# Optimization experiments

Measured on AMD Instinct MI355X. Metric: run time of the kernel, lower is better.

## Reference

```python
import jax, jax.numpy as jnp
import numpy as np

T, H, I, E, TOP_K = 1024, 2048, 1024, 32, 2
ROUTED_SCALING = 1.0


def setup_inputs() -> dict:
    key = jax.random.key(0)
    k0, k1, k2, k3, k4 = jax.random.split(key, 5)
    scale_h = 1.0 / np.sqrt(H)
    scale_i = 1.0 / np.sqrt(I)
    return {
        "x": jax.random.normal(k0, (T, H), dtype=jnp.float32),
        "gate_w": jax.random.normal(k1, (E, H), dtype=jnp.float32) * scale_h,      # router: Linear(H, E, bias=False)
        "gate_proj_w": jax.random.normal(k2, (E, I, H), dtype=jnp.float32) * scale_h,
        "up_proj_w": jax.random.normal(k3, (E, I, H), dtype=jnp.float32) * scale_h,
        "down_proj_w": jax.random.normal(k4, (E, H, I), dtype=jnp.float32) * scale_i,
    }


def reference(x, gate_w, gate_proj_w, up_proj_w, down_proj_w):
    # Router: logits [T, E] -> softmax -> top-k -> renormalize over selected experts
    logits = jnp.einsum("th,eh->te", x, gate_w)
    probs = jax.nn.softmax(logits, axis=-1)
    topk_vals, topk_idx = jax.lax.top_k(probs, TOP_K)            # [T, K]
    topk_w = topk_vals / jnp.sum(topk_vals, axis=-1, keepdims=True)
    topk_w = topk_w * ROUTED_SCALING
    # Dense combine weights [T, E]: zero for unselected experts
    onehot = jax.nn.one_hot(topk_idx, E, dtype=x.dtype)          # [T, K, E]
    combine = jnp.einsum("tk,tke->te", topk_w, onehot)           # [T, E]
    # Expert SwiGLU MLP computed densely, masked/weighted by combine weights
    g = jnp.einsum("th,eih->tei", x, gate_proj_w)                # [T, E, I]
    u = jnp.einsum("th,eih->tei", x, up_proj_w)                  # [T, E, I]
    h = jax.nn.silu(g) * u                                        # [T, E, I]
    h = h * combine[:, :, None]                                   # weight before down_proj
    out = jnp.einsum("tei,ehi->th", h, down_proj_w)              # [T, H]
    return out
```

## Files before the change

### kernel.cpp

```cpp
#include <hip/hip_runtime.h>
#include <hip/hip_bf16.h>

#define T_TOK 1024
#define H_DIM 2048
#define I_DIM 1024
#define NE 32

typedef __attribute__((ext_vector_type(8))) short bf16x8_t;
typedef __attribute__((ext_vector_type(4))) float f32x4_t;

__device__ __forceinline__ unsigned short f2bf(float f) {
    unsigned int u = __builtin_bit_cast(unsigned int, f);
    u += 0x7fffu + ((u >> 16) & 1u);
    return (unsigned short)(u >> 16);
}

__device__ __forceinline__ ushort4 f42bf(float4 v) {
    ushort4 r; r.x = f2bf(v.x); r.y = f2bf(v.y); r.z = f2bf(v.z); r.w = f2bf(v.w);
    return r;
}

__global__ __launch_bounds__(256) void moe_router(
    const float* __restrict__ x, const float* __restrict__ gwr,
    int* __restrict__ counts, int* __restrict__ etok, float* __restrict__ ew)
{
    const int t = blockIdx.x;
    const int e = threadIdx.x >> 3;
    const int j = threadIdx.x & 7;
    const float* xr = x + (size_t)t * H_DIM;
    const float* wr = gwr + (size_t)e * H_DIM;
    double s = 0.0;
    for (int c = j * 4; c < H_DIM; c += 32) {
        float4 a = *(const float4*)(xr + c);
        float4 b = *(const float4*)(wr + c);
        s += (double)a.x * b.x + (double)a.y * b.y + (double)a.z * b.z + (double)a.w * b.w;
    }
    s += __shfl_down(s, 4, 8);
    s += __shfl_down(s, 2, 8);
    s += __shfl_down(s, 1, 8);
    __shared__ float lg[NE];
    if (j == 0) lg[e] = (float)s;
    __syncthreads();
    if (threadIdx.x == 0) {
        float l1 = -1e30f, l2 = -1e30f; int i1 = 0, i2 = 0;
        for (int k = 0; k < NE; k++) {
            float v = lg[k];
            if (v > l1) { l2 = l1; i2 = i1; l1 = v; i1 = k; }
            else if (v > l2) { l2 = v; i2 = k; }
        }
        float w2 = 1.f / (1.f + __expf(l1 - l2));
        float w1 = 1.f - w2;
        int p1 = atomicAdd(&counts[i1], 1);
        etok[i1 * T_TOK + p1] = (t << 1);
        ew[i1 * T_TOK + p1] = w1;
        int p2 = atomicAdd(&counts[i2], 1);
        etok[i2 * T_TOK + p2] = (t << 1) | 1;
        ew[i2 * T_TOK + p2] = w2;
    }
}

__global__ __launch_bounds__(512, 2) void moe_gateup(
    const float* __restrict__ x,
    const float* __restrict__ gw,
    const float* __restrict__ uw,
    const int* __restrict__ counts,
    const int* __restrict__ etok,
    const float* __restrict__ ew,
    unsigned short* __restrict__ hbuf)
{
    __shared__ __align__(16) unsigned char smem[67584];
    unsigned short* As = (unsigned short*)smem;
    unsigned short* Gs = (unsigned short*)(smem + 18432);
    unsigned short* Us = (unsigned short*)(smem + 36864);
    float* GL = (float*)smem;

    const int e   = blockIdx.y;
    const int i0  = blockIdx.x * 128;
    const int cnt = counts[e];
    const int tid = threadIdx.x;
    const int wid = tid >> 6, lane = tid & 63;
    const int wm = wid >> 2, wn = wid & 3;
    const int lrow = lane & 15, quad = lane >> 4;

    const unsigned short* Bsrc = (wn < 2) ? Gs : Us;
    const int bro = (wn & 1) * 64;

    for (int m0 = 0; m0 < cnt; m0 += 128) {
        f32x4_t acc[4][4];
        #pragma unroll
        for (int a = 0; a < 4; a++)
            #pragma unroll
            for (int b = 0; b < 4; b++) acc[a][b] = (f32x4_t){0.f, 0.f, 0.f, 0.f};

        for (int k0 = 0; k0 < H_DIM; k0 += 64) {
            __syncthreads();
            #pragma unroll
            for (int i = 0; i < 4; i++) {
                int idx = tid + i * 512;
                int row = idx >> 4, c4 = idx & 15;
                int m = m0 + row;
                int tok = (m < cnt) ? (etok[e * T_TOK + m] >> 1) : 0;
                float4 v = *(const float4*)(x + (size_t)tok * H_DIM + k0 + c4 * 4);
                *(ushort4*)(As + row * 72 + c4 * 4) = f42bf(v);
            }
            #pragma unroll
            for (int i = 0; i < 4; i++) {
                int idx = tid + i * 512;
                int row = idx >> 4, c4 = idx & 15;
                float4 v = *(const float4*)(gw + ((size_t)e * I_DIM + i0 + row) * H_DIM + k0 + c4 * 4);
                *(ushort4*)(Gs + row * 72 + c4 * 4) = f42bf(v);
            }
            #pragma unroll
            for (int i = 0; i < 4; i++) {
                int idx = tid + i * 512;
                int row = idx >> 4, c4 = idx & 15;
                float4 v = *(const float4*)(uw + ((size_t)e * I_DIM + i0 + row) * H_DIM + k0 + c4 * 4);
                *(ushort4*)(Us + row * 72 + c4 * 4) = f42bf(v);
            }
            __syncthreads();
            #pragma unroll
            for (int kk = 0; kk < 2; kk++) {
                bf16x8_t af[4], bfr[4];
                #pragma unroll
                for (int q = 0; q < 4; q++)
                    af[q] = *(const bf16x8_t*)(As + (wm * 64 + q * 16 + lrow) * 72 + kk * 32 + quad * 8);
                #pragma unroll
                for (int q = 0; q < 4; q++)
                    bfr[q] = *(const bf16x8_t*)(Bsrc + (bro + q * 16 + lrow) * 72 + kk * 32 + quad * 8);
                #pragma unroll
                for (int a = 0; a < 4; a++)
                    #pragma unroll
                    for (int b = 0; b < 4; b++)
                        acc[a][b] = __builtin_amdgcn_mfma_f32_16x16x32_bf16(af[a], bfr[b], acc[a][b], 0, 0, 0);
            }
        }
        __syncthreads();
        if (wn < 2) {
            #pragma unroll
            for (int a = 0; a < 4; a++)
                #pragma unroll
                for (int b = 0; b < 4; b++)
                    #pragma unroll
                    for (int r = 0; r < 4; r++) {
                        int row = wm * 64 + a * 16 + quad * 4 + r;
                        int col = wn * 64 + b * 16 + lrow;
                        GL[row * 132 + col] = acc[a][b][r];
                    }
        }
        __syncthreads();
        if (wn >= 2) {
            #pragma unroll
            for (int a = 0; a < 4; a++)
                #pragma unroll
                for (int r = 0; r < 4; r++) {
                    int row = wm * 64 + a * 16 + quad * 4 + r;
                    int m = m0 + row;
                    if (m < cnt) {
                        int ent = etok[e * T_TOK + m];
                        float w = ew[e * T_TOK + m];
                        #pragma unroll
                        for (int b = 0; b < 4; b++) {
                            int colI = (wn - 2) * 64 + b * 16 + lrow;
                            float g = GL[row * 132 + colI];
                            float u = acc[a][b][r];
                            float hv = g / (1.f + __expf(-g)) * u * w;
                            hbuf[(size_t)ent * I_DIM + i0 + colI] = f2bf(hv);
                        }
                    }
                }
        }
    }
}

__global__ __launch_bounds__(512, 2) void moe_down(
    const unsigned short* __restrict__ hbuf,
    const float* __restrict__ dw,
    const int* __restrict__ counts,
    const int* __restrict__ etok,
    float* __restrict__ out)
{
    __shared__ __align__(16) unsigned char smem[55296];
    unsigned short* As = (unsigned short*)smem;
    unsigned short* Ds = (unsigned short*)(smem + 18432);

    const int e   = blockIdx.y;
    const int n0  = blockIdx.x * 256;
    const int cnt = counts[e];
    const int tid = threadIdx.x;
    const int wid = tid >> 6, lane = tid & 63;
    const int wm = wid >> 2, wn = wid & 3;
    const int lrow = lane & 15, quad = lane >> 4;

    for (int m0 = 0; m0 < cnt; m0 += 128) {
        f32x4_t acc[4][4];
        #pragma unroll
        for (int a = 0; a < 4; a++)
            #pragma unroll
            for (int b = 0; b < 4; b++) acc[a][b] = (f32x4_t){0.f, 0.f, 0.f, 0.f};

        for (int k0 = 0; k0 < I_DIM; k0 += 64) {
            __syncthreads();
            #pragma unroll
            for (int i = 0; i < 2; i++) {
                int idx = tid + i * 512;
                int row = idx >> 3, c8 = idx & 7;
                int m = m0 + row;
                int ent = (m < cnt) ? etok[e * T_TOK + m] : 0;
                uint4 v = *(const uint4*)(hbuf + (size_t)ent * I_DIM + k0 + c8 * 8);
                *(uint4*)(As + row * 72 + c8 * 8) = v;
            }
            #pragma unroll
            for (int i = 0; i < 8; i++) {
                int idx = tid + i * 512;
                int row = idx >> 4, c4 = idx & 15;
                float4 v = *(const float4*)(dw + ((size_t)e * H_DIM + n0 + row) * I_DIM + k0 + c4 * 4);
                *(ushort4*)(Ds + row * 72 + c4 * 4) = f42bf(v);
            }
            __syncthreads();
            #pragma unroll
            for (int kk = 0; kk < 2; kk++) {
                bf16x8_t af[4], bfr[4];
                #pragma unroll
                for (int q = 0; q < 4; q++)
                    af[q] = *(const bf16x8_t*)(As + (wm * 64 + q * 16 + lrow) * 72 + kk * 32 + quad * 8);
                #pragma unroll
                for (int q = 0; q < 4; q++)
                    bfr[q] = *(const bf16x8_t*)(Ds + (wn * 64 + q * 16 + lrow) * 72 + kk * 32 + quad * 8);
                #pragma unroll
                for (int a = 0; a < 4; a++)
                    #pragma unroll
                    for (int b = 0; b < 4; b++)
                        acc[a][b] = __builtin_amdgcn_mfma_f32_16x16x32_bf16(af[a], bfr[b], acc[a][b], 0, 0, 0);
            }
        }
        #pragma unroll
        for (int a = 0; a < 4; a++)
            #pragma unroll
            for (int r = 0; r < 4; r++) {
                int row = wm * 64 + a * 16 + quad * 4 + r;
                int m = m0 + row;
                if (m < cnt) {
                    int tok = etok[e * T_TOK + m] >> 1;
                    float* orow = out + (size_t)tok * H_DIM + n0 + wn * 64;
                    #pragma unroll
                    for (int b = 0; b < 4; b++)
                        atomicAdd(orow + b * 16 + lrow, acc[a][b][r]);
                }
            }
    }
}

extern "C" void kernel_launch(void* const* d_in, const int* in_sizes, int n_in,
                              void* d_out, int out_size, void* d_ws, size_t ws_size,
                              hipStream_t stream) {
    const float* x   = (const float*)d_in[0];
    const float* gwr = (const float*)d_in[1];
    const float* gw  = (const float*)d_in[2];
    const float* uw  = (const float*)d_in[3];
    const float* dw  = (const float*)d_in[4];
    float* out = (float*)d_out;

    char* ws = (char*)d_ws;
    int*   counts = (int*)ws;
    int*   etok   = (int*)(ws + 4096);
    float* ew     = (float*)(ws + 4096 + 131072);
    unsigned short* hbuf = (unsigned short*)(ws + 4096 + 262144);

    hipMemsetAsync(counts, 0, 128, stream);
    hipMemsetAsync(d_out, 0, (size_t)out_size * sizeof(float), stream);

    moe_router<<<T_TOK, 256, 0, stream>>>(x, gwr, counts, etok, ew);
    moe_gateup<<<dim3(I_DIM / 128, NE), 512, 0, stream>>>(x, gw, uw, counts, etok, ew, hbuf);
    moe_down<<<dim3(H_DIM / 256, NE), 512, 0, stream>>>(hbuf, dw, counts, etok, out);
}
```

Measured before the change: 882.0 us.

## Double-buffer MoE GEMM tiles with register prefetch and halve tile width

Both expert GEMM kernels now prefetch the next K-slice into registers while MFMAs run on the current LDS buffer, then convert and store into an alternate LDS buffer, using one barrier per step. Tile widths are halved (64 intermediate columns for gate/up, 128 hidden columns for down), which doubles the grid and gives better CU coverage. The aim is to hide global load latency and raise occupancy in this bandwidth-bound workload. In exchange, activation rows are re-read by more blocks, and larger LDS plus tighter launch bounds may raise register pressure.

Measured after the change: 828.0 us. 6.1% less time.

```diff
diff --git a/kernel.cpp b/kernel.cpp
--- a/kernel.cpp
+++ b/kernel.cpp
@@ -59,7 +59,7 @@
     }
 }
 
-__global__ __launch_bounds__(512, 2) void moe_gateup(
+__global__ __launch_bounds__(512, 4) void moe_gateup(
     const float* __restrict__ x,
     const float* __restrict__ gw,
     const float* __restrict__ uw,
@@ -68,183 +68,213 @@
     const float* __restrict__ ew,
     unsigned short* __restrict__ hbuf)
 {
-    __shared__ __align__(16) unsigned char smem[67584];
-    unsigned short* As = (unsigned short*)smem;
-    unsigned short* Gs = (unsigned short*)(smem + 18432);
-    unsigned short* Us = (unsigned short*)(smem + 36864);
-    float* GL = (float*)smem;
-
+    __shared__ __align__(16) unsigned char smem[73728];
     const int e   = blockIdx.y;
-    const int i0  = blockIdx.x * 128;
+    const int i0  = blockIdx.x * 64;
     const int cnt = counts[e];
     const int tid = threadIdx.x;
     const int wid = tid >> 6, lane = tid & 63;
-    const int wm = wid >> 2, wn = wid & 3;
+    const int wm = wid >> 1, wn = wid & 1;
     const int lrow = lane & 15, quad = lane >> 4;
 
-    const unsigned short* Bsrc = (wn < 2) ? Gs : Us;
-    const int bro = (wn & 1) * 64;
+    const float* gbase = gw + ((size_t)e * I_DIM + i0 + (tid >> 4)) * H_DIM + (tid & 15) * 4;
+    const float* ubase = uw + ((size_t)e * I_DIM + i0 + (tid >> 4)) * H_DIM + (tid & 15) * 4;
 
     for (int m0 = 0; m0 < cnt; m0 += 128) {
-        f32x4_t acc[4][4];
-        #pragma unroll
-        for (int a = 0; a < 4; a++)
-            #pragma unroll
-            for (int b = 0; b < 4; b++) acc[a][b] = (f32x4_t){0.f, 0.f, 0.f, 0.f};
-
-        for (int k0 = 0; k0 < H_DIM; k0 += 64) {
+        const float* arow[4];
+        #pragma unroll
+        for (int i = 0; i < 4; i++) {
+            int idx = tid + i * 512;
+            int m = m0 + (idx >> 4);
+            int tok = (m < cnt) ? (etok[e * T_TOK + m] >> 1) : 0;
+            arow[i] = x + (size_t)tok * H_DIM + (idx & 15) * 4;
+        }
+
+        f32x4_t acc[2][4];
+        #pragma unroll
+        for (int a = 0; a < 2; a++)
+            #pragma unroll
+            for (int c = 0; c < 4; c++) acc[a][c] = (f32x4_t){0.f, 0.f, 0.f, 0.f};
+
+        float4 ra[4], rg[2], ru[2];
+        auto load_t = [&](int k0) {
+            #pragma unroll
+            for (int i = 0; i < 4; i++) ra[i] = *(const float4*)(arow[i] + k0);
+            #pragma unroll
+            for (int i = 0; i < 2; i++) rg[i] = *(const float4*)(gbase + (size_t)i * 32 * H_DIM + k0);
+            #pragma unroll
+            for (int i = 0; i < 2; i++) ru[i] = *(const float4*)(ubase + (size_t)i * 32 * H_DIM + k0);
+        };
+        auto store_t = [&](int b) {
+            unsigned short* As = (unsigned short*)(smem + b * 36864);
+            unsigned short* Gs = As + 9216;
+            unsigned short* Us = As + 13824;
+            #pragma unroll
+            for (int i = 0; i < 4; i++) { int idx = tid + i * 512; *(ushort4*)(As + (idx >> 4) * 72 + (idx & 15) * 4) = f42bf(ra[i]); }
+            #pragma unroll
+            for (int i = 0; i < 2; i++) { int idx = tid + i * 512; *(ushort4*)(Gs + (idx >> 4) * 72 + (idx & 15) * 4) = f42bf(rg[i]); }
+            #pragma unroll
+            for (int i = 0; i < 2; i++) { int idx = tid + i * 512; *(ushort4*)(Us + (idx >> 4) * 72 + (idx & 15) * 4) = f42bf(ru[i]); }
+        };
+        auto mm = [&](int b) {
+            const unsigned short* As = (const unsigned short*)(smem + b * 36864);
+            const unsigned short* Bs = As + 9216 + wn * 4608;
+            #pragma unroll
+            for (int kk = 0; kk < 2; kk++) {
+                bf16x8_t af[2], bfr[4];
+                #pragma unroll
+                for (int q = 0; q < 2; q++)
+                    af[q] = *(const bf16x8_t*)(As + (wm * 32 + q * 16 + lrow) * 72 + kk * 32 + quad * 8);
+                #pragma unroll
+                for (int q = 0; q < 4; q++)
+                    bfr[q] = *(const bf16x8_t*)(Bs + (q * 16 + lrow) * 72 + kk * 32 + quad * 8);
+                #pragma unroll
+                for (int a = 0; a < 2; a++)
+                    #pragma unroll
+                    for (int c = 0; c < 4; c++)
+                        acc[a][c] = __builtin_amdgcn_mfma_f32_16x16x32_bf16(af[a], bfr[c], acc[a][c], 0, 0, 0);
+            }
+        };
+
+        load_t(0);
+        store_t(0);
+        __syncthreads();
+        for (int k = 0; k < 32; k++) {
+            if (k < 31) load_t((k + 1) * 64);
+            mm(k & 1);
+            if (k < 31) store_t((k + 1) & 1);
             __syncthreads();
-            #pragma unroll
-            for (int i = 0; i < 4; i++) {
-                int idx = tid + i * 512;
-                int row = idx >> 4, c4 = idx & 15;
-                int m = m0 + row;
-                int tok = (m < cnt) ? (etok[e * T_TOK + m] >> 1) : 0;
-                float4 v = *(const float4*)(x + (size_t)tok * H_DIM + k0 + c4 * 4);
-                *(ushort4*)(As + row * 72 + c4 * 4) = f42bf(v);
-            }
-            #pragma unroll
-            for (int i = 0; i < 4; i++) {
-                int idx = tid + i * 512;
-                int row = idx >> 4, c4 = idx & 15;
-                float4 v = *(const float4*)(gw + ((size_t)e * I_DIM + i0 + row) * H_DIM + k0 + c4 * 4);
-                *(ushort4*)(Gs + row * 72 + c4 * 4) = f42bf(v);
-            }
-            #pragma unroll
-            for (int i = 0; i < 4; i++) {
-                int idx = tid + i * 512;
-                int row = idx >> 4, c4 = idx & 15;
-                float4 v = *(const float4*)(uw + ((size_t)e * I_DIM + i0 + row) * H_DIM + k0 + c4 * 4);
-                *(ushort4*)(Us + row * 72 + c4 * 4) = f42bf(v);
-            }
-            __syncthreads();
-            #pragma unroll
-            for (int kk = 0; kk < 2; kk++) {
-                bf16x8_t af[4], bfr[4];
-                #pragma unroll
-                for (int q = 0; q < 4; q++)
-                    af[q] = *(const bf16x8_t*)(As + (wm * 64 + q * 16 + lrow) * 72 + kk * 32 + quad * 8);
-                #pragma unroll
-                for (int q = 0; q < 4; q++)
-                    bfr[q] = *(const bf16x8_t*)(Bsrc + (bro + q * 16 + lrow) * 72 + kk * 32 + quad * 8);
-                #pragma unroll
-                for (int a = 0; a < 4; a++)
-                    #pragma unroll
-                    for (int b = 0; b < 4; b++)
-                        acc[a][b] = __builtin_amdgcn_mfma_f32_16x16x32_bf16(af[a], bfr[b], acc[a][b], 0, 0, 0);
-            }
-        }
-        __syncthreads();
-        if (wn < 2) {
-            #pragma unroll
-            for (int a = 0; a < 4; a++)
-                #pragma unroll
-                for (int b = 0; b < 4; b++)
+        }
+
+        float* GL = (float*)smem;
+        if (wn == 0) {
+            #pragma unroll
+            for (int a = 0; a < 2; a++)
+                #pragma unroll
+                for (int c = 0; c < 4; c++)
                     #pragma unroll
                     for (int r = 0; r < 4; r++) {
-                        int row = wm * 64 + a * 16 + quad * 4 + r;
-                        int col = wn * 64 + b * 16 + lrow;
-                        GL[row * 132 + col] = acc[a][b][r];
+                        int row = wm * 32 + a * 16 + quad * 4 + r;
+                        GL[row * 68 + c * 16 + lrow] = acc[a][c][r];
                     }
         }
         __syncthreads();
-        if (wn >= 2) {
-            #pragma unroll
-            for (int a = 0; a < 4; a++)
+        if (wn == 1) {
+            #pragma unroll
+            for (int a = 0; a < 2; a++)
                 #pragma unroll
                 for (int r = 0; r < 4; r++) {
-                    int row = wm * 64 + a * 16 + quad * 4 + r;
+                    int row = wm * 32 + a * 16 + quad * 4 + r;
                     int m = m0 + row;
                     if (m < cnt) {
                         int ent = etok[e * T_TOK + m];
                         float w = ew[e * T_TOK + m];
                         #pragma unroll
-                        for (int b = 0; b < 4; b++) {
-                            int colI = (wn - 2) * 64 + b * 16 + lrow;
-                            float g = GL[row * 132 + colI];
-                            float u = acc[a][b][r];
+                        for (int c = 0; c < 4; c++) {
+                            int colI = c * 16 + lrow;
+                            float g = GL[row * 68 + colI];
+                            float u = acc[a][c][r];
                             float hv = g / (1.f + __expf(-g)) * u * w;
                             hbuf[(size_t)ent * I_DIM + i0 + colI] = f2bf(hv);
                         }
                     }
                 }
         }
+        __syncthreads();
     }
 }
 
-__global__ __launch_bounds__(512, 2) void moe_down(
+__global__ __launch_bounds__(512, 4) void moe_down(
     const unsigned short* __restrict__ hbuf,
     const float* __restrict__ dw,
     const int* __restrict__ counts,
     const int* __restrict__ etok,
     float* __restrict__ out)
 {
-    __shared__ __align__(16) unsigned char smem[55296];
-    unsigned short* As = (unsigned short*)smem;
-    unsigned short* Ds = (unsigned short*)(smem + 18432);
-
+    __shared__ __align__(16) unsigned char smem[73728];
     const int e   = blockIdx.y;
-    const int n0  = blockIdx.x * 256;
+    const int n0  = blockIdx.x * 128;
     const int cnt = counts[e];
     const int tid = threadIdx.x;
     const int wid = tid >> 6, lane = tid & 63;
-    const int wm = wid >> 2, wn = wid & 3;
+    const int wm = wid >> 1, wn = wid & 1;
     const int lrow = lane & 15, quad = lane >> 4;
 
+    const float* dbase = dw + ((size_t)e * H_DIM + n0 + (tid >> 4)) * I_DIM + (tid & 15) * 4;
+
     for (int m0 = 0; m0 < cnt; m0 += 128) {
-        f32x4_t acc[4][4];
-        #pragma unroll
-        for (int a = 0; a < 4; a++)
-            #pragma unroll
-            for (int b = 0; b < 4; b++) acc[a][b] = (f32x4_t){0.f, 0.f, 0.f, 0.f};
-
-        for (int k0 = 0; k0 < I_DIM; k0 += 64) {
-            __syncthreads();
-            #pragma unroll
-            for (int i = 0; i < 2; i++) {
-                int idx = tid + i * 512;
-                int row = idx >> 3, c8 = idx & 7;
-                int m = m0 + row;
-                int ent = (m < cnt) ? etok[e * T_TOK + m] : 0;
-                uint4 v = *(const uint4*)(hbuf + (size_t)ent * I_DIM + k0 + c8 * 8);
-                *(uint4*)(As + row * 72 + c8 * 8) = v;
-            }
-            #pragma unroll
-            for (int i = 0; i < 8; i++) {
-                int idx = tid + i * 512;
-                int row = idx >> 4, c4 = idx & 15;
-                float4 v = *(const float4*)(dw + ((size_t)e * H_DIM + n0 + row) * I_DIM + k0 + c4 * 4);
-                *(ushort4*)(Ds + row * 72 + c4 * 4) = f42bf(v);
-            }
-            __syncthreads();
+        const unsigned short* arow[2];
+        #pragma unroll
+        for (int i = 0; i < 2; i++) {
+            int idx = tid + i * 512;
+            int m = m0 + (idx >> 3);
+            int ent = (m < cnt) ? etok[e * T_TOK + m] : 0;
+            arow[i] = hbuf + (size_t)ent * I_DIM + (idx & 7) * 8;
+        }
+
+        f32x4_t acc[2][4];
+        #pragma unroll
+        for (int a = 0; a < 2; a++)
+            #pragma unroll
+            for (int c = 0; c < 4; c++) acc[a][c] = (f32x4_t){0.f, 0.f, 0.f, 0.f};
+
+        uint4 raa[2]; float4 rd[4];
+        auto load_t = [&](int k0) {
+            #pragma unroll
+            for (int i = 0; i < 2; i++) raa[i] = *(const uint4*)(arow[i] + k0);
+            #pragma unroll
+            for (int i = 0; i < 4; i++) rd[i] = *(const float4*)(dbase + (size_t)i * 32 * I_DIM + k0);
+        };
+        auto store_t = [&](int b) {
+            unsigned short* As = (unsigned short*)(smem + b * 36864);
+            unsigned short* Ds = As + 9216;
+            #pragma unroll
+            for (int i = 0; i < 2; i++) { int idx = tid + i * 512; *(uint4*)(As + (idx >> 3) * 72 + (idx & 7) * 8) = raa[i]; }
+            #pragma unroll
+            for (int i = 0; i < 4; i++) { int idx = tid + i * 512; *(ushort4*)(Ds + (idx >> 4) * 72 + (idx & 15) * 4) = f42bf(rd[i]); }
+        };
+        auto mm = [&](int b) {
+            const unsigned short* As = (const unsigned short*)(smem + b * 36864);
+            const unsigned short* Ds = As + 9216;
             #pragma unroll
             for (int kk = 0; kk < 2; kk++) {
-                bf16x8_t af[4], bfr[4];
-                #pragma unroll
-                for (int q = 0; q < 4; q++)
-                    af[q] = *(const bf16x8_t*)(As + (wm * 64 + q * 16 + lrow) * 72 + kk * 32 + quad * 8);
+                bf16x8_t af[2], bfr[4];
+                #pragma unroll
+                for (int q = 0; q < 2; q++)
+                    af[q] = *(const bf16x8_t*)(As + (wm * 32 + q * 16 + lrow) * 72 + kk * 32 + quad * 8);
                 #pragma unroll
                 for (int q = 0; q < 4; q++)
                     bfr[q] = *(const bf16x8_t*)(Ds + (wn * 64 + q * 16 + lrow) * 72 + kk * 32 + quad * 8);
                 #pragma unroll
-                for (int a = 0; a < 4; a++)
+                for (int a = 0; a < 2; a++)
                     #pragma unroll
-                    for (int b = 0; b < 4; b++)
-                        acc[a][b] = __builtin_amdgcn_mfma_f32_16x16x32_bf16(af[a], bfr[b], acc[a][b], 0, 0, 0);
+                    for (int c = 0; c < 4; c++)
+                        acc[a][c] = __builtin_amdgcn_mfma_f32_16x16x32_bf16(af[a], bfr[c], acc[a][c], 0, 0, 0);
             }
-        }
-        #pragma unroll
-        for (int a = 0; a < 4; a++)
+        };
+
+        load_t(0);
+        store_t(0);
+        __syncthreads();
+        for (int k = 0; k < 16; k++) {
+            if (k < 15) load_t((k + 1) * 64);
+            mm(k & 1);
+            if (k < 15) store_t((k + 1) & 1);
+            __syncthreads();
+        }
+
+        #pragma unroll
+        for (int a = 0; a < 2; a++)
             #pragma unroll
             for (int r = 0; r < 4; r++) {
-                int row = wm * 64 + a * 16 + quad * 4 + r;
+                int row = wm * 32 + a * 16 + quad * 4 + r;
                 int m = m0 + row;
                 if (m < cnt) {
                     int tok = etok[e * T_TOK + m] >> 1;
                     float* orow = out + (size_t)tok * H_DIM + n0 + wn * 64;
                     #pragma unroll
-                    for (int b = 0; b < 4; b++)
-                        atomicAdd(orow + b * 16 + lrow, acc[a][b][r]);
+                    for (int c = 0; c < 4; c++)
+                        atomicAdd(orow + c * 16 + lrow, acc[a][c][r]);
                 }
             }
     }
@@ -270,6 +300,6 @@
     hipMemsetAsync(d_out, 0, (size_t)out_size * sizeof(float), stream);
 
     moe_router<<<T_TOK, 256, 0, stream>>>(x, gwr, counts, etok, ew);
-    moe_gateup<<<dim3(I_DIM / 128, NE), 512, 0, stream>>>(x, gw, uw, counts, etok, ew, hbuf);
-    moe_down<<<dim3(H_DIM / 256, NE), 512, 0, stream>>>(hbuf, dw, counts, etok, out);
-}
+    moe_gateup<<<dim3(I_DIM / 64, NE), 512, 0, stream>>>(x, gw, uw, counts, etok, ew, hbuf);
+    moe_down<<<dim3(H_DIM / 128, NE), 512, 0, stream>>>(hbuf, dw, counts, etok, out);
+}
```
